# Kernel optimization log

Hardware: AMD Instinct MI355X
Metric: run time of the kernel (lower is better)

Reference implementation:

```python
import jax, jax.numpy as jnp
import numpy as np

N = 100_000      # nodes
E = 1_600_000    # edges
D_IN = 128       # input_dim
H = 128          # hidden_dim
L = 3            # num_layers
G = 128          # graphs in batch
EPS = 1e-5       # BatchNorm1d eps


def setup_inputs() -> dict:
    key = jax.random.key(0)
    ks = jax.random.split(key, 8)
    inp = {
        "x": jax.random.normal(ks[0], (N, D_IN), dtype=jnp.float32),
        "edge_index": jax.random.randint(ks[1], (2, E), 0, N),
        "batch": jnp.sort(jax.random.randint(ks[2], (N,), 0, G)),
    }
    for i in range(L):
        din = D_IN if i == 0 else H
        kw = jax.random.fold_in(key, 100 + i)
        inp[f"W{i}"] = jax.random.normal(kw, (din, H), dtype=jnp.float32) / np.sqrt(din).astype(np.float32)
        inp[f"b{i}"] = jnp.zeros((H,), jnp.float32)
        inp[f"g{i}"] = jnp.ones((H,), jnp.float32)
        inp[f"beta{i}"] = jnp.zeros((H,), jnp.float32)
    return inp


def _gcn_conv(x, W, b, src, dst, dinv):
    # GCNConv (normalize=True, add_self_loops=True):
    # out = D^{-1/2} (A + I) D^{-1/2} X W + b, deg computed on dst with self-loops
    h = x @ W                                   # [N,H]
    coef = (dinv[src] * dinv[dst])[:, None]     # per-edge norm
    agg = jax.ops.segment_sum(h[src] * coef, dst, num_segments=N)
    agg = agg + h * (dinv * dinv)[:, None]      # self-loop term deg^{-1}
    return agg + b


def _batchnorm(z, g, beta):
    mu = jnp.mean(z, axis=0)
    var = jnp.mean(jnp.square(z - mu), axis=0)  # biased var (training-mode BN)
    return (z - mu) * jax.lax.rsqrt(var + EPS) * g + beta


def reference(x, edge_index, batch,
              W0, b0, g0, beta0,
              W1, b1, g1, beta1,
              W2, b2, g2, beta2):
    src, dst = edge_index[0], edge_index[1]
    # degree of A + I on target index
    deg = jax.ops.segment_sum(jnp.ones((E,), x.dtype), dst, num_segments=N) + 1.0
    dinv = jax.lax.rsqrt(deg)
    params = [(W0, b0, g0, beta0), (W1, b1, g1, beta1), (W2, b2, g2, beta2)]
    zs = []
    h = x
    for (W, b, g, beta) in params:
        h = _gcn_conv(h, W, b, src, dst, dinv)
        h = jax.nn.relu(h)
        h = _batchnorm(h, g, beta)
        zs.append(h)
    pooled = [jax.ops.segment_sum(z, batch, num_segments=G) for z in zs]  # sum pool
    h_cat = jnp.concatenate(zs, axis=1)        # [N, L*H]
    g_cat = jnp.concatenate(pooled, axis=1)    # [G, L*H]
    return h_cat, g_cat
```

## Files before the change

### kernel.cpp

```cpp
#include <hip/hip_runtime.h>

#define NN 100000
#define NE 1600000
#define NG 128
#define BN_EPS 1e-5f
#define NBKT 64
#define AGG_BLOCKS 2048
#define AGG_WAVES (AGG_BLOCKS * 4)
#define NBUCK 98
#define BIN_BLOCKS 256
#define BIN_CHUNK 6250

typedef short s16x8 __attribute__((ext_vector_type(8)));
typedef float f32x4 __attribute__((ext_vector_type(4)));

static __device__ __forceinline__ unsigned short f2bf(float f) {
    unsigned u = __float_as_uint(f);
    u += 0x7fffu + ((u >> 16) & 1u);
    return (unsigned short)(u >> 16);
}
static __device__ __forceinline__ unsigned packbf(float a, float b) {
    return (unsigned)f2bf(a) | ((unsigned)f2bf(b) << 16);
}
static __device__ __forceinline__ float bf_lo(unsigned u) { return __uint_as_float(u << 16); }
static __device__ __forceinline__ float bf_hi(unsigned u) { return __uint_as_float(u & 0xffff0000u); }
static __device__ __forceinline__ float bf2f(ushort u) { return __uint_as_float((unsigned)u << 16); }

__global__ __launch_bounds__(256) void k_bhist(const int* __restrict__ dst, int* __restrict__ gbh) {
    __shared__ int lh[128];
    int t = threadIdx.x;
    if (t < 128) lh[t] = 0;
    __syncthreads();
    for (int e = blockIdx.x * 256 + t; e < NE; e += gridDim.x * 256)
        atomicAdd(&lh[dst[e] >> 10], 1);
    __syncthreads();
    if (t < 128 && lh[t]) atomicAdd(&gbh[t], lh[t]);
}

__global__ __launch_bounds__(128) void k_bscan(const int* __restrict__ gbh, int* __restrict__ gbase,
                                               int* __restrict__ gcur, int* __restrict__ row_start) {
    __shared__ int s[128];
    int t = threadIdx.x;
    int v = gbh[t];
    s[t] = v;
    __syncthreads();
    for (int o = 1; o < 128; o <<= 1) {
        int a = (t >= o) ? s[t - o] : 0;
        __syncthreads();
        s[t] += a;
        __syncthreads();
    }
    int ex = s[t] - v;
    gbase[t] = ex;
    gcur[t] = ex;
    if (t == 127) { gbase[128] = s[127]; row_start[NN] = NE; }
}

__global__ __launch_bounds__(256) void k_bin(const int* __restrict__ src, const int* __restrict__ dst,
                                             int* __restrict__ gcur, int* __restrict__ tmp) {
    __shared__ int lh[128], lb[128], lc[128];
    int t = threadIdx.x;
    if (t < 128) lh[t] = 0;
    __syncthreads();
    int e0 = blockIdx.x * BIN_CHUNK, e1 = e0 + BIN_CHUNK;
    for (int e = e0 + t; e < e1; e += 256) atomicAdd(&lh[dst[e] >> 10], 1);
    __syncthreads();
    if (t < 128) {
        int c = lh[t];
        lb[t] = c ? atomicAdd(&gcur[t], c) : 0;
        lc[t] = 0;
    }
    __syncthreads();
    for (int e = e0 + t; e < e1; e += 256) {
        int d = dst[e];
        int b = d >> 10;
        int off = atomicAdd(&lc[b], 1);
        tmp[lb[b] + off] = (src[e] << 10) | (d & 1023);
    }
}

__global__ __launch_bounds__(256) void k_csr(const int* __restrict__ tmp, const int* __restrict__ gbase,
                                             int* __restrict__ esrc, int* __restrict__ row_start,
                                             float* __restrict__ dinv) {
    __shared__ int h[1024], hs[1024], part[256];
    int b = blockIdx.x, t = threadIdx.x;
    int base = gbase[b], end = gbase[b + 1];
#pragma unroll
    for (int k = 0; k < 4; ++k) h[t * 4 + k] = 0;
    __syncthreads();
    for (int i = base + t; i < end; i += 256) atomicAdd(&h[tmp[i] & 1023], 1);
    __syncthreads();
    int l0 = h[t * 4], l1 = h[t * 4 + 1], l2 = h[t * 4 + 2], l3 = h[t * 4 + 3];
    int ssum = l0 + l1 + l2 + l3;
    part[t] = ssum;
    __syncthreads();
    for (int o = 1; o < 256; o <<= 1) {
        int a = (t >= o) ? part[t - o] : 0;
        __syncthreads();
        part[t] += a;
        __syncthreads();
    }
    int ex = part[t] - ssum;
    hs[t * 4]     = ex;
    hs[t * 4 + 1] = ex + l0;
    hs[t * 4 + 2] = ex + l0 + l1;
    hs[t * 4 + 3] = ex + l0 + l1 + l2;
    int n0 = b * 1024 + t * 4;
#pragma unroll
    for (int k = 0; k < 4; ++k) {
        int n = n0 + k;
        if (n < NN) {
            row_start[n] = base + hs[t * 4 + k];
            dinv[n] = rsqrtf((float)h[t * 4 + k] + 1.0f);
        }
    }
    __syncthreads();
    for (int i = base + t; i < end; i += 256) {
        int rec = tmp[i];
        int pos = atomicAdd(&hs[rec & 1023], 1);
        esrc[base + pos] = rec >> 10;
    }
}

__global__ __launch_bounds__(256) void k_cast(const float* __restrict__ x, uint4* __restrict__ xb) {
    int i = blockIdx.x * 256 + threadIdx.x;
    if (i >= NN * 16) return;
    float4 a = *(const float4*)(x + (size_t)i * 8);
    float4 b = *(const float4*)(x + (size_t)i * 8 + 4);
    uint4 o;
    o.x = packbf(a.x, a.y);
    o.y = packbf(a.z, a.w);
    o.z = packbf(b.x, b.y);
    o.w = packbf(b.z, b.w);
    xb[i] = o;
}

__global__ __launch_bounds__(64) void k_wfrag(const float* __restrict__ W, ushort* __restrict__ Wf) {
    int unit = blockIdx.x;
    int lane = threadIdx.x;
    int ks = unit >> 3, nb = unit & 7;
    int n = nb * 16 + (lane & 15);
    int k0 = ks * 32 + (lane >> 4) * 8;
    ushort o[8];
#pragma unroll
    for (int j = 0; j < 8; ++j) o[j] = f2bf(W[(size_t)(k0 + j) * 128 + n]);
    ushort* p = Wf + ((size_t)unit * 64 + lane) * 8;
#pragma unroll
    for (int j = 0; j < 8; ++j) p[j] = o[j];
}

__global__ __launch_bounds__(128) void k_finwscale(const float* __restrict__ S, const float* __restrict__ Q,
                                                   const float* __restrict__ gam, const float* __restrict__ bet,
                                                   float* __restrict__ svec, float* __restrict__ tvec,
                                                   const float* __restrict__ Wnext, float* __restrict__ tW,
                                                   const ushort* __restrict__ Wfb, ushort* __restrict__ Wff) {
    int bid = blockIdx.x;
    int t = threadIdx.x;
    if (bid == 0) {
        __shared__ float ts[128];
        float s = 0.f, q = 0.f;
        for (int k = 0; k < NBKT; ++k) {
            s += S[k * 128 + t];
            q += Q[k * 128 + t];
        }
        float mean = s / (float)NN;
        float var = q / (float)NN - mean * mean;
        float rstd = rsqrtf(fmaxf(var, 0.f) + BN_EPS);
        float sc = gam[t] * rstd;
        float sh = bet[t] - mean * sc;
        svec[t] = sc;
        tvec[t] = sh;
        ts[t] = sh;
        __syncthreads();
        if (Wnext) {
            float acc = 0.f;
            for (int k = 0; k < 128; ++k) acc += ts[k] * Wnext[(size_t)k * 128 + t];
            tW[t] = acc;
        }
    } else {
        __shared__ float sv[32];
        int unit = bid - 1;
        int kbase = (unit >> 3) * 32;
        if (t < 32) {
            int c = kbase + t;
            float s = 0.f, q = 0.f;
            for (int k = 0; k < NBKT; ++k) {
                s += S[k * 128 + c];
                q += Q[k * 128 + c];
            }
            float mean = s / (float)NN;
            float var = q / (float)NN - mean * mean;
            sv[t] = gam[c] * rsqrtf(fmaxf(var, 0.f) + BN_EPS);
        }
        __syncthreads();
        if (t < 64) {
            int ko = (t >> 4) * 8;
            const ushort* p = Wfb + ((size_t)unit * 64 + t) * 8;
            ushort* o = Wff + ((size_t)unit * 64 + t) * 8;
#pragma unroll
            for (int j = 0; j < 8; ++j) o[j] = f2bf(bf2f(p[j]) * sv[ko + j]);
        }
    }
}

__global__ __launch_bounds__(256) void k_gemm(const ushort* __restrict__ Xb, const ushort* __restrict__ Wf,
                                              const float* __restrict__ tW, const float* __restrict__ dinv,
                                              ushort* __restrict__ hm, const float* __restrict__ svec,
                                              const float* __restrict__ tvec, float* __restrict__ outp,
                                              int lofs) {
    int tid = threadIdx.x;
    int wid = tid >> 6, lane = tid & 63;
    int r0 = blockIdx.x * 64 + wid * 16;
    int m = lane & 15, g = lane >> 4;
    int xrow = r0 + m;
    int xr = (xrow < NN) ? xrow : (NN - 1);
    const ushort* Xrow = Xb + (size_t)xr * 128 + g * 8;
    s16x8 af[4];
#pragma unroll
    for (int ks = 0; ks < 4; ++ks) af[ks] = *(const s16x8*)(Xrow + ks * 32);
    f32x4 acc[8];
#pragma unroll
    for (int nb = 0; nb < 8; ++nb) acc[nb] = (f32x4){0.f, 0.f, 0.f, 0.f};
#pragma unroll
    for (int ks = 0; ks < 4; ++ks) {
#pragma unroll
        for (int nb = 0; nb < 8; ++nb) {
            s16x8 wf = *(const s16x8*)(Wf + ((size_t)(ks * 8 + nb) * 64 + lane) * 8);
            acc[nb] = __builtin_amdgcn_mfma_f32_16x16x32_bf16(wf, af[ks], acc[nb], 0, 0, 0);
        }
    }
    if (xrow < NN) {
        float ds = dinv[xr];
        ushort* orow = hm + (size_t)xrow * 128 + g * 4;
        if (tW) {
#pragma unroll
            for (int nb = 0; nb < 8; ++nb) {
                float4 tw = *(const float4*)(tW + nb * 16 + g * 4);
                ushort4 o;
                o.x = f2bf(ds * (acc[nb][0] + tw.x));
                o.y = f2bf(ds * (acc[nb][1] + tw.y));
                o.z = f2bf(ds * (acc[nb][2] + tw.z));
                o.w = f2bf(ds * (acc[nb][3] + tw.w));
                *(ushort4*)(orow + nb * 16) = o;
            }
        } else {
#pragma unroll
            for (int nb = 0; nb < 8; ++nb) {
                ushort4 o;
                o.x = f2bf(ds * acc[nb][0]);
                o.y = f2bf(ds * acc[nb][1]);
                o.z = f2bf(ds * acc[nb][2]);
                o.w = f2bf(ds * acc[nb][3]);
                *(ushort4*)(orow + nb * 16) = o;
            }
        }
        if (svec) {
            float* zrow = outp + (size_t)xrow * 384 + lofs;
#pragma unroll
            for (int ks = 0; ks < 4; ++ks) {
                int c0 = ks * 32 + g * 8;
                float4 s0 = *(const float4*)(svec + c0);
                float4 s1 = *(const float4*)(svec + c0 + 4);
                float4 t0 = *(const float4*)(tvec + c0);
                float4 t1 = *(const float4*)(tvec + c0 + 4);
                float4 z0, z1;
                z0.x = bf2f((ushort)af[ks][0]) * s0.x + t0.x;
                z0.y = bf2f((ushort)af[ks][1]) * s0.y + t0.y;
                z0.z = bf2f((ushort)af[ks][2]) * s0.z + t0.z;
                z0.w = bf2f((ushort)af[ks][3]) * s0.w + t0.w;
                z1.x = bf2f((ushort)af[ks][4]) * s1.x + t1.x;
                z1.y = bf2f((ushort)af[ks][5]) * s1.y + t1.y;
                z1.z = bf2f((ushort)af[ks][6]) * s1.z + t1.z;
                z1.w = bf2f((ushort)af[ks][7]) * s1.w + t1.w;
                *(float4*)(zrow + c0) = z0;
                *(float4*)(zrow + c0 + 4) = z1;
            }
        }
    }
}

__global__ __launch_bounds__(256) void k_agg(const uint* __restrict__ hm32, const int* __restrict__ esrc,
                                             const int* __restrict__ rs, const float* __restrict__ dinv,
                                             const float* __restrict__ bias, uint* __restrict__ act,
                                             float* __restrict__ bnsum, float* __restrict__ bnsq) {
    __shared__ float ls[128], lq[128];
    int tid = threadIdx.x;
    if (tid < 128) { ls[tid] = 0.f; lq[tid] = 0.f; }
    __syncthreads();
    int lane = tid & 63;
    int wgid = blockIdx.x * 4 + (tid >> 6);
    float2 b2 = *(const float2*)(bias + lane * 2);
    float s0 = 0.f, s1 = 0.f, q0 = 0.f, q1 = 0.f;

    for (int n = wgid; n < NN; n += AGG_WAVES) {
        uint self = hm32[(size_t)n * 64 + lane];
        float a0 = bf_lo(self);
        float a1 = bf_hi(self);

        int i  = __builtin_amdgcn_readfirstlane(rs[n]);
        int i1 = __builtin_amdgcn_readfirstlane(rs[n + 1]);

        int idxv = 0;
        if (i < i1) idxv = esrc[i + min(min(lane, 15), i1 - i - 1)];

        while (i < i1) {
            int cnt = i1 - i;
            cnt = (cnt > 16) ? 16 : cnt;
            int cur = idxv;
            int inext = i + cnt;
            if (inext < i1)
                idxv = esrc[inext + min(min(lane, 15), i1 - inext - 1)];
            uint g[16];
#pragma unroll
            for (int u = 0; u < 16; ++u) {
                int sidx = __builtin_amdgcn_readlane(cur, u);
                sidx = (u < cnt) ? sidx : NN;
                g[u] = hm32[(size_t)sidx * 64 + lane];
            }
#pragma unroll
            for (int u = 0; u < 16; ++u) {
                a0 += bf_lo(g[u]);
                a1 += bf_hi(g[u]);
            }
            i = inext;
        }
        float di = dinv[n];
        float z0 = fmaxf(fmaf(di, a0, b2.x), 0.f);
        float z1 = fmaxf(fmaf(di, a1, b2.y), 0.f);
        act[(size_t)n * 64 + lane] = packbf(z0, z1);
        s0 += z0; s1 += z1;
        q0 += z0 * z0; q1 += z1 * z1;
    }
    atomicAdd(&ls[lane * 2],     s0);
    atomicAdd(&ls[lane * 2 + 1], s1);
    atomicAdd(&lq[lane * 2],     q0);
    atomicAdd(&lq[lane * 2 + 1], q1);
    __syncthreads();
    if (tid < 128) {
        int bkt = blockIdx.x & (NBKT - 1);
        atomicAdd(&bnsum[bkt * 128 + tid], ls[tid]);
        atomicAdd(&bnsq[bkt * 128 + tid],  lq[tid]);
    }
}

__global__ __launch_bounds__(128) void k_pool(const uint* __restrict__ act32, const float* __restrict__ svec,
                                              const float* __restrict__ tvec, const int* __restrict__ batch,
                                              float* __restrict__ gout, int lofs) {
    int t = threadIdx.x;
    int lane = t & 63;
    int w = t >> 6;
    int n0 = blockIdx.x * 64;
    float sc0 = svec[lane * 2], sc1 = svec[lane * 2 + 1];
    float sh0 = tvec[lane * 2], sh1 = tvec[lane * 2 + 1];
    float s0 = 0.f, s1 = 0.f;
    int cnt = 0, curg = -1;
    for (int k = w; k < 64; k += 2) {
        int n = n0 + k;
        if (n >= NN) break;
        int gn = batch[n];
        if (gn != curg) {
            if (cnt) {
                atomicAdd(&gout[(size_t)curg * 384 + lofs + lane * 2],     sc0 * s0 + sh0 * (float)cnt);
                atomicAdd(&gout[(size_t)curg * 384 + lofs + lane * 2 + 1], sc1 * s1 + sh1 * (float)cnt);
            }
            curg = gn; s0 = 0.f; s1 = 0.f; cnt = 0;
        }
        uint v = act32[(size_t)n * 64 + lane];
        s0 += bf_lo(v);
        s1 += bf_hi(v);
        ++cnt;
    }
    if (cnt) {
        atomicAdd(&gout[(size_t)curg * 384 + lofs + lane * 2],     sc0 * s0 + sh0 * (float)cnt);
        atomicAdd(&gout[(size_t)curg * 384 + lofs + lane * 2 + 1], sc1 * s1 + sh1 * (float)cnt);
    }
}

__global__ __launch_bounds__(128) void k_norm2(const ushort* __restrict__ act, const float* __restrict__ svec,
                                               const float* __restrict__ tvec, float* __restrict__ outp) {
    int c = threadIdx.x;
    int n0 = blockIdx.x * 64;
    if (n0 >= NN) return;
    int n1 = n0 + 64; if (n1 > NN) n1 = NN;
    float scale = svec[c];
    float shift = tvec[c];
    for (int n = n0; n < n1; ++n)
        outp[(size_t)n * 384 + 256 + c] = bf2f(act[(size_t)n * 128 + c]) * scale + shift;
}

extern "C" void kernel_launch(void* const* d_in, const int* in_sizes, int n_in,
                              void* d_out, int out_size, void* d_ws, size_t ws_size,
                              hipStream_t stream) {
    const float* x = (const float*)d_in[0];
    const int* ei = (const int*)d_in[1];
    const int* src = ei;
    const int* dst = ei + NE;
    const int* batch = (const int*)d_in[2];
    const float *W[3], *b[3], *g[3], *beta[3];
    for (int l = 0; l < 3; ++l) {
        W[l]    = (const float*)d_in[3 + 4 * l];
        b[l]    = (const float*)d_in[4 + 4 * l];
        g[l]    = (const float*)d_in[5 + 4 * l];
        beta[l] = (const float*)d_in[6 + 4 * l];
    }
    float* out = (float*)d_out;
    float* gout = out + (size_t)NN * 384;

    char* ws = (char*)d_ws;
    size_t off = 0;
    auto alloc = [&](size_t bytes) -> char* {
        off = (off + 255) & ~(size_t)255;
        char* p = ws + off;
        off += bytes;
        return p;
    };
    ushort* xb       = (ushort*)alloc((size_t)NN * 256);
    ushort* act      = (ushort*)alloc((size_t)NN * 256);
    ushort* hm       = (ushort*)alloc((size_t)(NN + 1) * 256);
    int*    esrc     = (int*)alloc((size_t)NE * 4);
    int*    tmp      = (int*)alloc((size_t)NE * 4);
    int*    row_start= (int*)alloc((size_t)(NN + 1) * 4);
    float*  dinv     = (float*)alloc((size_t)NN * 4);
    float*  bnst     = (float*)alloc((size_t)3 * 2 * NBKT * 128 * 4);
    ushort* Wf       = (ushort*)alloc(3 * 16384 * 2);
    ushort* Wff      = (ushort*)alloc(16384 * 2);
    float*  svt      = (float*)alloc(3 * 2 * 128 * 4);
    float*  tW       = (float*)alloc(128 * 4);
    int*    misc     = (int*)alloc(512 * 4);
    int* gbh   = misc;
    int* gbase = misc + 128;
    int* gcur  = misc + 384;
    (void)ws_size;

    hipMemsetAsync(gbh, 0, 128 * 4, stream);
    hipMemsetAsync(hm + (size_t)NN * 128, 0, 256, stream);
    hipMemsetAsync(bnst, 0, (size_t)3 * 2 * NBKT * 128 * 4, stream);
    hipMemsetAsync(gout, 0, (size_t)NG * 384 * 4, stream);

    k_bhist<<<512, 256, 0, stream>>>(dst, gbh);
    k_bscan<<<1, 128, 0, stream>>>(gbh, gbase, gcur, row_start);
    k_bin<<<BIN_BLOCKS, 256, 0, stream>>>(src, dst, gcur, tmp);
    k_csr<<<NBUCK, 256, 0, stream>>>(tmp, gbase, esrc, row_start, dinv);
    k_cast<<<(NN * 16 + 255) / 256, 256, 0, stream>>>(x, (uint4*)xb);
    for (int l = 0; l < 3; ++l) k_wfrag<<<32, 64, 0, stream>>>(W[l], Wf + l * 16384);

    for (int l = 0; l < 3; ++l) {
        float* S = bnst + (size_t)l * 2 * NBKT * 128;
        float* Q = S + NBKT * 128;
        float* sv = svt + l * 256;
        float* tv = sv + 128;
        const ushort* gin = (l == 0) ? xb : act;
        const ushort* wfrag = (l == 0) ? (Wf + 0) : Wff;
        const float* tw_in = (l == 0) ? nullptr : tW;
        const float* psv = (l == 0) ? nullptr : (svt + (l - 1) * 256);
        const float* ptv = (l == 0) ? nullptr : (svt + (l - 1) * 256 + 128);

        k_gemm<<<(NN + 63) / 64, 256, 0, stream>>>(gin, wfrag, tw_in, dinv, hm,
                                                   psv, ptv, out, (l - 1) * 128);
        k_agg<<<AGG_BLOCKS, 256, 0, stream>>>((const uint*)hm, esrc, row_start, dinv, b[l],
                                              (uint*)act, S, Q);
        k_finwscale<<<(l < 2) ? 33 : 1, 128, 0, stream>>>(S, Q, g[l], beta[l], sv, tv,
                                                          (l < 2) ? W[l + 1] : nullptr, tW,
                                                          (l < 2) ? (Wf + (l + 1) * 16384) : nullptr, Wff);
        k_pool<<<(NN + 63) / 64, 128, 0, stream>>>((const uint*)act, sv, tv, batch, gout, l * 128);
    }
    k_norm2<<<(NN + 63) / 64, 128, 0, stream>>>(act, svt + 2 * 256, svt + 2 * 256 + 128, out);
}
```

Before: 507.5 us.

## Fold input cast into GEMM and BN output writes into pooling kernel

The separate fp32-to-bf16 cast kernel is removed, and the layer-0 GEMM now reads fp32 x and converts it in registers. The normalized per-layer output write moves out of the next layer's GEMM and the final k_norm2 kernel into k_pool, which already reads act. The three weight-fragment launches are merged into one. The aim is fewer launches and less redundant traffic: no bf16 copy of x is written and read back, and act is not reread for the final layer. In exchange, layer-0 GEMM loads twice the input bytes, and k_pool now carries the full 384-wide output write.

Result: faster. 460.9 us (-9.2%).

```diff
diff --git a/kernel.cpp b/kernel.cpp
--- a/kernel.cpp
+++ b/kernel.cpp
@@ -122,21 +122,11 @@
     }
 }
 
-__global__ __launch_bounds__(256) void k_cast(const float* __restrict__ x, uint4* __restrict__ xb) {
-    int i = blockIdx.x * 256 + threadIdx.x;
-    if (i >= NN * 16) return;
-    float4 a = *(const float4*)(x + (size_t)i * 8);
-    float4 b = *(const float4*)(x + (size_t)i * 8 + 4);
-    uint4 o;
-    o.x = packbf(a.x, a.y);
-    o.y = packbf(a.z, a.w);
-    o.z = packbf(b.x, b.y);
-    o.w = packbf(b.z, b.w);
-    xb[i] = o;
-}
-
-__global__ __launch_bounds__(64) void k_wfrag(const float* __restrict__ W, ushort* __restrict__ Wf) {
-    int unit = blockIdx.x;
+__global__ __launch_bounds__(64) void k_wfrag(const float* __restrict__ W0, const float* __restrict__ W1,
+                                              const float* __restrict__ W2, ushort* __restrict__ Wf) {
+    int layer = blockIdx.x >> 5;
+    int unit = blockIdx.x & 31;
+    const float* W = (layer == 0) ? W0 : ((layer == 1) ? W1 : W2);
     int lane = threadIdx.x;
     int ks = unit >> 3, nb = unit & 7;
     int n = nb * 16 + (lane & 15);
@@ -144,7 +134,7 @@
     ushort o[8];
 #pragma unroll
     for (int j = 0; j < 8; ++j) o[j] = f2bf(W[(size_t)(k0 + j) * 128 + n]);
-    ushort* p = Wf + ((size_t)unit * 64 + lane) * 8;
+    ushort* p = Wf + (size_t)layer * 16384 + ((size_t)unit * 64 + lane) * 8;
 #pragma unroll
     for (int j = 0; j < 8; ++j) p[j] = o[j];
 }
@@ -203,21 +193,34 @@
     }
 }
 
-__global__ __launch_bounds__(256) void k_gemm(const ushort* __restrict__ Xb, const ushort* __restrict__ Wf,
-                                              const float* __restrict__ tW, const float* __restrict__ dinv,
-                                              ushort* __restrict__ hm, const float* __restrict__ svec,
-                                              const float* __restrict__ tvec, float* __restrict__ outp,
-                                              int lofs) {
+__global__ __launch_bounds__(256) void k_gemm(const ushort* __restrict__ Xb, const float* __restrict__ xf32,
+                                              const ushort* __restrict__ Wf, const float* __restrict__ tW,
+                                              const float* __restrict__ dinv, ushort* __restrict__ hm) {
     int tid = threadIdx.x;
     int wid = tid >> 6, lane = tid & 63;
     int r0 = blockIdx.x * 64 + wid * 16;
     int m = lane & 15, g = lane >> 4;
     int xrow = r0 + m;
     int xr = (xrow < NN) ? xrow : (NN - 1);
-    const ushort* Xrow = Xb + (size_t)xr * 128 + g * 8;
     s16x8 af[4];
-#pragma unroll
-    for (int ks = 0; ks < 4; ++ks) af[ks] = *(const s16x8*)(Xrow + ks * 32);
+    if (xf32) {
+        const float* Xr = xf32 + (size_t)xr * 128 + g * 8;
+#pragma unroll
+        for (int ks = 0; ks < 4; ++ks) {
+            float4 a = *(const float4*)(Xr + ks * 32);
+            float4 b = *(const float4*)(Xr + ks * 32 + 4);
+            s16x8 v;
+            v[0] = (short)f2bf(a.x); v[1] = (short)f2bf(a.y);
+            v[2] = (short)f2bf(a.z); v[3] = (short)f2bf(a.w);
+            v[4] = (short)f2bf(b.x); v[5] = (short)f2bf(b.y);
+            v[6] = (short)f2bf(b.z); v[7] = (short)f2bf(b.w);
+            af[ks] = v;
+        }
+    } else {
+        const ushort* Xrow = Xb + (size_t)xr * 128 + g * 8;
+#pragma unroll
+        for (int ks = 0; ks < 4; ++ks) af[ks] = *(const s16x8*)(Xrow + ks * 32);
+    }
     f32x4 acc[8];
 #pragma unroll
     for (int nb = 0; nb < 8; ++nb) acc[nb] = (f32x4){0.f, 0.f, 0.f, 0.f};
@@ -254,28 +257,6 @@
                 *(ushort4*)(orow + nb * 16) = o;
             }
         }
-        if (svec) {
-            float* zrow = outp + (size_t)xrow * 384 + lofs;
-#pragma unroll
-            for (int ks = 0; ks < 4; ++ks) {
-                int c0 = ks * 32 + g * 8;
-                float4 s0 = *(const float4*)(svec + c0);
-                float4 s1 = *(const float4*)(svec + c0 + 4);
-                float4 t0 = *(const float4*)(tvec + c0);
-                float4 t1 = *(const float4*)(tvec + c0 + 4);
-                float4 z0, z1;
-                z0.x = bf2f((ushort)af[ks][0]) * s0.x + t0.x;
-                z0.y = bf2f((ushort)af[ks][1]) * s0.y + t0.y;
-                z0.z = bf2f((ushort)af[ks][2]) * s0.z + t0.z;
-                z0.w = bf2f((ushort)af[ks][3]) * s0.w + t0.w;
-                z1.x = bf2f((ushort)af[ks][4]) * s1.x + t1.x;
-                z1.y = bf2f((ushort)af[ks][5]) * s1.y + t1.y;
-                z1.z = bf2f((ushort)af[ks][6]) * s1.z + t1.z;
-                z1.w = bf2f((ushort)af[ks][7]) * s1.w + t1.w;
-                *(float4*)(zrow + c0) = z0;
-                *(float4*)(zrow + c0 + 4) = z1;
-            }
-        }
     }
 }
 
@@ -345,7 +326,7 @@
 
 __global__ __launch_bounds__(128) void k_pool(const uint* __restrict__ act32, const float* __restrict__ svec,
                                               const float* __restrict__ tvec, const int* __restrict__ batch,
-                                              float* __restrict__ gout, int lofs) {
+                                              float* __restrict__ gout, float* __restrict__ outp, int lofs) {
     int t = threadIdx.x;
     int lane = t & 63;
     int w = t >> 6;
@@ -366,26 +347,19 @@
             curg = gn; s0 = 0.f; s1 = 0.f; cnt = 0;
         }
         uint v = act32[(size_t)n * 64 + lane];
-        s0 += bf_lo(v);
-        s1 += bf_hi(v);
+        float a0 = bf_lo(v), a1 = bf_hi(v);
+        float2 z;
+        z.x = a0 * sc0 + sh0;
+        z.y = a1 * sc1 + sh1;
+        *(float2*)(outp + (size_t)n * 384 + lofs + lane * 2) = z;
+        s0 += a0;
+        s1 += a1;
         ++cnt;
     }
     if (cnt) {
         atomicAdd(&gout[(size_t)curg * 384 + lofs + lane * 2],     sc0 * s0 + sh0 * (float)cnt);
         atomicAdd(&gout[(size_t)curg * 384 + lofs + lane * 2 + 1], sc1 * s1 + sh1 * (float)cnt);
     }
-}
-
-__global__ __launch_bounds__(128) void k_norm2(const ushort* __restrict__ act, const float* __restrict__ svec,
-                                               const float* __restrict__ tvec, float* __restrict__ outp) {
-    int c = threadIdx.x;
-    int n0 = blockIdx.x * 64;
-    if (n0 >= NN) return;
-    int n1 = n0 + 64; if (n1 > NN) n1 = NN;
-    float scale = svec[c];
-    float shift = tvec[c];
-    for (int n = n0; n < n1; ++n)
-        outp[(size_t)n * 384 + 256 + c] = bf2f(act[(size_t)n * 128 + c]) * scale + shift;
 }
 
 extern "C" void kernel_launch(void* const* d_in, const int* in_sizes, int n_in,
@@ -414,7 +388,6 @@
         off += bytes;
         return p;
     };
-    ushort* xb       = (ushort*)alloc((size_t)NN * 256);
     ushort* act      = (ushort*)alloc((size_t)NN * 256);
     ushort* hm       = (ushort*)alloc((size_t)(NN + 1) * 256);
     int*    esrc     = (int*)alloc((size_t)NE * 4);
@@ -441,28 +414,24 @@
     k_bscan<<<1, 128, 0, stream>>>(gbh, gbase, gcur, row_start);
     k_bin<<<BIN_BLOCKS, 256, 0, stream>>>(src, dst, gcur, tmp);
     k_csr<<<NBUCK, 256, 0, stream>>>(tmp, gbase, esrc, row_start, dinv);
-    k_cast<<<(NN * 16 + 255) / 256, 256, 0, stream>>>(x, (uint4*)xb);
-    for (int l = 0; l < 3; ++l) k_wfrag<<<32, 64, 0, stream>>>(W[l], Wf + l * 16384);
+    k_wfrag<<<96, 64, 0, stream>>>(W[0], W[1], W[2], Wf);
 
     for (int l = 0; l < 3; ++l) {
         float* S = bnst + (size_t)l * 2 * NBKT * 128;
         float* Q = S + NBKT * 128;
         float* sv = svt + l * 256;
         float* tv = sv + 128;
-        const ushort* gin = (l == 0) ? xb : act;
+        const ushort* gin = (l == 0) ? (const ushort*)nullptr : act;
+        const float* xin = (l == 0) ? x : nullptr;
         const ushort* wfrag = (l == 0) ? (Wf + 0) : Wff;
         const float* tw_in = (l == 0) ? nullptr : tW;
-        const float* psv = (l == 0) ? nullptr : (svt + (l - 1) * 256);
-        const float* ptv = (l == 0) ? nullptr : (svt + (l - 1) * 256 + 128);
-
-        k_gemm<<<(NN + 63) / 64, 256, 0, stream>>>(gin, wfrag, tw_in, dinv, hm,
-                                                   psv, ptv, out, (l - 1) * 128);
+
+        k_gemm<<<(NN + 63) / 64, 256, 0, stream>>>(gin, xin, wfrag, tw_in, dinv, hm);
         k_agg<<<AGG_BLOCKS, 256, 0, stream>>>((const uint*)hm, esrc, row_start, dinv, b[l],
                                               (uint*)act, S, Q);
         k_finwscale<<<(l < 2) ? 33 : 1, 128, 0, stream>>>(S, Q, g[l], beta[l], sv, tv,
                                                           (l < 2) ? W[l + 1] : nullptr, tW,
                                                           (l < 2) ? (Wf + (l + 1) * 16384) : nullptr, Wff);
-        k_pool<<<(NN + 63) / 64, 128, 0, stream>>>((const uint*)act, sv, tv, batch, gout, l * 128);
-    }
-    k_norm2<<<(NN + 63) / 64, 128, 0, stream>>>(act, svt + 2 * 256, svt + 2 * 256 + 128, out);
-}
+        k_pool<<<(NN + 63) / 64, 128, 0, stream>>>((const uint*)act, sv, tv, batch, gout, out, l * 128);
+    }
+}
```
